# Kernel optimization log

Hardware: AMD Instinct MI355X
Metric: run time of the kernel (lower is better)

## Reference

```python
import jax, jax.numpy as jnp
import numpy as np
from jax import lax

K = 16
SIGMA2 = 1.0  # sigma=1.0 squared
EPS = 1e-06


def setup_inputs() -> dict:
    key = jax.random.key(0)
    xyz = jax.random.normal(key, (4, 3, 4096), dtype=jnp.float32)
    return {"xyz": xyz}


def reference(xyz):
    # xyz: (B, 3, N)
    B, _, N = xyz.shape
    pts = jnp.transpose(xyz, (0, 2, 1))  # (B, N, 3)

    sq = jnp.sum(pts * pts, axis=-1)  # (B, N)
    d2 = sq[:, :, None] + sq[:, None, :] - 2.0 * jnp.einsum("bnd,bmd->bnm", pts, pts)

    # k nearest neighbors (smallest distance, includes self like torch knn on same set)
    _, idx = lax.top_k(-d2, K)  # idx: (B, N, K)

    # gather neighbor coordinates and recompute exact squared distance (faithful to source)
    neighbors = jax.vmap(lambda p, i: p[i])(pts, idx)  # (B, N, K, 3)
    diff = pts[:, :, None, :] - neighbors
    dist2 = jnp.sum(diff * diff, axis=-1)  # (B, N, K)
    weights = jnp.exp(-dist2 / (2.0 * SIGMA2))

    # scatter k-sparse weights into dense adjacency (topk indices per row are unique)
    bb = jnp.arange(B)[:, None, None]
    ii = jnp.arange(N)[None, :, None]
    A = jnp.zeros((B, N, N), dtype=xyz.dtype).at[bb, ii, idx].set(weights)
    A = 0.5 * (A + jnp.swapaxes(A, 1, 2))

    # symmetric normalized Laplacian L = I - D^{-1/2} A D^{-1/2} (diag scaling via broadcast)
    D = jnp.clip(jnp.sum(A, axis=-1), EPS, None)
    d_is = D ** -0.5  # (B, N)
    L = jnp.eye(N, dtype=xyz.dtype)[None] - d_is[:, :, None] * A * d_is[:, None, :]
    return L
```

## Files before the change

kernel.cpp:

```cpp
#include <hip/hip_runtime.h>
#include <math.h>

#pragma clang fp contract(off)

#define NPTS 4096
#define KNN  16
#define RPBK 32
#define KT   1024
#define CAP  128
#define CAPIN 64
#define SPILLCAP 262144
#define RROWS 4

__device__ __forceinline__ unsigned okey(float f) {
    f = f + 0.0f;
    unsigned u = __float_as_uint(f);
    return u ^ (((unsigned)((int)u >> 31)) | 0x80000000u);
}

__device__ __forceinline__ unsigned long long wmin64(unsigned long long v) {
    for (int o = 32; o > 0; o >>= 1) { unsigned long long w = __shfl_xor(v, o); v = w < v ? w : v; }
    return v;
}

__global__ void zero_kernel(float* __restrict__ p, int n) {
    int i = blockIdx.x * blockDim.x + threadIdx.x;
    if (i < n) p[i] = 0.0f;
}

__device__ __forceinline__ float thresh16(float k, int lane) {
    int rank = 0;
    for (int s = 0; s < 64; ++s) {
        float ks = __shfl(k, s);
        rank += (ks < k || (ks == k && s < lane)) ? 1 : 0;
    }
    unsigned long long m = __ballot(rank == 15);
    return __shfl(k, __ffsll(m) - 1);
}

__device__ __forceinline__ int select16(const float4* __restrict__ spts,
                                        const int* __restrict__ list,
                                        int cnt, float4 P, int lane) {
    if (cnt <= 64) {
        float key = __builtin_huge_valf();
        int m = -1;
        if (lane < cnt) {
            m = list[lane];
            float4 Q = spts[m];
            float dot = (P.x * Q.x + P.y * Q.y) + P.z * Q.z;
            key = (P.w + Q.w) - 2.0f * dot;
        }
        int rank = 0;
        for (int s = 0; s < 64; ++s) {
            float ks = __shfl(key, s);
            rank += (ks < key || (ks == key && s < lane)) ? 1 : 0;
        }
        return __builtin_amdgcn_ds_permute(rank << 2, m);
    }
    if (cnt <= CAP) {
        unsigned long long e0 = ~0ull, e1 = ~0ull;
        if (lane < cnt) {
            int m = list[lane]; float4 Q = spts[m];
            float dot = (P.x * Q.x + P.y * Q.y) + P.z * Q.z;
            float d2  = (P.w + Q.w) - 2.0f * dot;
            e0 = ((unsigned long long)okey(d2) << 32) | (unsigned)m;
        }
        if (lane + 64 < cnt) {
            int m = list[lane + 64]; float4 Q = spts[m];
            float dot = (P.x * Q.x + P.y * Q.y) + P.z * Q.z;
            float d2  = (P.w + Q.w) - 2.0f * dot;
            e1 = ((unsigned long long)okey(d2) << 32) | (unsigned)m;
        }
        int selm = -1;
        unsigned long long c = e0 < e1 ? e0 : e1;
        for (int r = 0; r < KNN; ++r) {
            unsigned long long mn = wmin64(c);
            if (c == mn) {
                if (e0 == mn) e0 = ~0ull; else e1 = ~0ull;
                c = e0 < e1 ? e0 : e1;
            }
            if (lane == r) selm = (int)(unsigned)(mn & 0xFFFFFFFFull);
        }
        return selm;
    }
    unsigned long long last = 0; int selm = -1;
    for (int r = 0; r < KNN; ++r) {
        unsigned long long bestp = ~0ull;
        for (int i = 0; i < NPTS / 64; ++i) {
            int m = i * 64 + lane;
            float4 Q  = spts[m];
            float dot = (P.x * Q.x + P.y * Q.y) + P.z * Q.z;
            float d2  = (P.w + Q.w) - 2.0f * dot;
            unsigned long long key = ((unsigned long long)okey(d2) << 32) | (unsigned)m;
            if (key > last && key < bestp) bestp = key;
        }
        unsigned long long mn = wmin64(bestp);
        if (lane == r) selm = (int)(unsigned)(mn & 0xFFFFFFFFull);
        last = mn;
    }
    return selm;
}

__device__ __forceinline__ void emit_row(int rowg, int b, int selm, float4 P,
                                         const float4* __restrict__ spts,
                                         float* __restrict__ Dsum,
                                         int* __restrict__ idx_out,
                                         float* __restrict__ w_out,
                                         int* __restrict__ cnt,
                                         int* __restrict__ inc,
                                         int* __restrict__ spillc,
                                         int* __restrict__ spill,
                                         int do_inc, int lane) {
    float wgt = 0.0f;
    if (lane < KNN) {
        int j = selm;
        float4 Q = spts[j];
        float dx = P.x - Q.x, dy = P.y - Q.y, dz = P.z - Q.z;
        float dist2 = (dx * dx + dy * dy) + dz * dz;
        wgt = expf(-(dist2 * 0.5f));
        size_t base = (size_t)rowg * KNN + lane;
        idx_out[base] = j;
        w_out[base]   = wgt;
        int jg = (b << 12) + j;
        atomicAdd(&Dsum[jg], 0.5f * wgt);
        if (do_inc) {
            int pos = atomicAdd(&cnt[jg], 1);
            if (pos < CAPIN) {
                inc[(size_t)jg * CAPIN + pos] = (int)base;
            } else {
                int sp = atomicAdd(spillc, 1);
                if (sp < SPILLCAP) spill[sp] = (int)base;
            }
        }
    }
    float rs = wgt;
    for (int o = 32; o > 0; o >>= 1) rs += __shfl_xor(rs, o);
    if (lane == 0) atomicAdd(&Dsum[rowg], 0.5f * rs);
}

__global__ __launch_bounds__(KT, 4) void knn_kernel(const float* __restrict__ xyz,
                                                    float* __restrict__ Dsum,
                                                    int* __restrict__ idx_out,
                                                    float* __restrict__ w_out,
                                                    int* __restrict__ cnt,
                                                    int* __restrict__ inc,
                                                    int* __restrict__ spillc,
                                                    int* __restrict__ spill,
                                                    int do_inc) {
    __shared__ float4 spts[NPTS];
    __shared__ int    lists[RPBK][CAP];

    const int t    = threadIdx.x;
    const int lane = t & 63;
    const int wv   = t >> 6;
    const int row0 = blockIdx.x * RPBK + 2 * wv;
    const int b    = row0 >> 12;
    const float* X = xyz + (size_t)b * 3 * NPTS;

    for (int i = t; i < NPTS; i += KT) {
        float x = X[i], y = X[NPTS + i], z = X[2 * NPTS + i];
        spts[i] = make_float4(x, y, z, (x * x + y * y) + z * z);
    }
    __syncthreads();

    const float4 PA = spts[row0 & (NPTS - 1)];
    const float4 PB = spts[(row0 + 1) & (NPTS - 1)];

    float bA = __builtin_huge_valf(), bB = __builtin_huge_valf();
    for (int i = 0; i < NPTS / 64; ++i) {
        float4 Q  = spts[i * 64 + lane];
        float dotA = (PA.x * Q.x + PA.y * Q.y) + PA.z * Q.z;
        float d2A  = (PA.w + Q.w) - 2.0f * dotA;
        float dotB = (PB.x * Q.x + PB.y * Q.y) + PB.z * Q.z;
        float d2B  = (PB.w + Q.w) - 2.0f * dotB;
        bA = fminf(bA, d2A);
        bB = fminf(bB, d2B);
    }
    const float TA = thresh16(bA, lane);
    const float TB = thresh16(bB, lane);

    int* listA = &lists[2 * wv][0];
    int* listB = &lists[2 * wv + 1][0];
    int cA = 0, cB = 0;
    for (int i = 0; i < NPTS / 64; ++i) {
        int m = i * 64 + lane;
        float4 Q  = spts[m];
        float dotA = (PA.x * Q.x + PA.y * Q.y) + PA.z * Q.z;
        float d2A  = (PA.w + Q.w) - 2.0f * dotA;
        float dotB = (PB.x * Q.x + PB.y * Q.y) + PB.z * Q.z;
        float d2B  = (PB.w + Q.w) - 2.0f * dotB;
        bool pA = d2A <= TA;
        unsigned long long balA = __ballot(pA);
        if (pA) {
            int pos = cA + __popcll(balA & ((1ull << lane) - 1ull));
            if (pos < CAP) listA[pos] = m;
        }
        cA += (int)__popcll(balA);
        bool pB = d2B <= TB;
        unsigned long long balB = __ballot(pB);
        if (pB) {
            int pos = cB + __popcll(balB & ((1ull << lane) - 1ull));
            if (pos < CAP) listB[pos] = m;
        }
        cB += (int)__popcll(balB);
    }

    int selA = select16(spts, listA, cA, PA, lane);
    int selB = select16(spts, listB, cB, PB, lane);
    emit_row(row0,     b, selA, PA, spts, Dsum, idx_out, w_out,
             cnt, inc, spillc, spill, do_inc, lane);
    emit_row(row0 + 1, b, selB, PB, spts, Dsum, idx_out, w_out,
             cnt, inc, spillc, spill, do_inc, lane);
}

__global__ void dis_kernel(const float* __restrict__ Dsum, float* __restrict__ dis, int n) {
    int i = blockIdx.x * blockDim.x + threadIdx.x;
    if (i < n) dis[i] = 1.0f / sqrtf(fmaxf(Dsum[i], 1e-6f));
}

__global__ __launch_bounds__(1024, 4) void row_kernel(const int* __restrict__ idxb,
                                                      const float* __restrict__ wb,
                                                      const float* __restrict__ dis,
                                                      const int* __restrict__ cnt,
                                                      const int* __restrict__ inc,
                                                      float* __restrict__ L) {
    __shared__ float row[RROWS * NPTS];
    const int r0 = blockIdx.x * RROWS;
    const int b  = r0 >> 12;

    float4* row4 = (float4*)row;
    for (int i = threadIdx.x; i < RROWS * NPTS / 4; i += 1024)
        row4[i] = make_float4(0.0f, 0.0f, 0.0f, 0.0f);
    __syncthreads();

    const int rr = threadIdx.x >> 8;
    const int tt = threadIdx.x & 255;
    const int r  = r0 + rr;
    float* myrow = row + rr * NPTS;
    const float dn = dis[r];

    if (tt < KNN) {
        int g = r * KNN + tt;
        int j = idxb[g];
        float v = -0.5f * wb[g] * dn * dis[(b << 12) + j];
        atomicAdd(&myrow[j], v);
    }

    int c = cnt[r];
    if (c > CAPIN) c = CAPIN;
    for (int i = tt; i < c; i += 256) {
        int g   = inc[(size_t)r * CAPIN + i];
        int src = g >> 4;
        float v = -0.5f * wb[g] * dis[src] * dn;
        atomicAdd(&myrow[src & (NPTS - 1)], v);
    }
    __syncthreads();

    const int n0 = r0 & (NPTS - 1);
    float4* Lr = (float4*)(L + (size_t)b * NPTS * NPTS + (size_t)n0 * NPTS);
    for (int q = threadIdx.x; q < RROWS * NPTS / 4; q += 1024) {
        float4 v = row4[q];
        int n = n0 + (q >> 10);
        if ((q & 1023) == (n >> 2)) ((float*)&v)[n & 3] += 1.0f;
        Lr[q] = v;
    }
}

__global__ __launch_bounds__(256) void spill_kernel(const int* __restrict__ spillc,
                                                    const int* __restrict__ spill,
                                                    const int* __restrict__ idxb,
                                                    const float* __restrict__ wb,
                                                    const float* __restrict__ dis,
                                                    float* __restrict__ L) {
    int c = spillc[0];
    if (c > SPILLCAP) c = SPILLCAP;
    for (int i = blockIdx.x * blockDim.x + threadIdx.x; i < c;
         i += gridDim.x * blockDim.x) {
        int g   = spill[i];
        int src = g >> 4;
        int b   = src >> 12;
        int nn  = src & (NPTS - 1);
        int j   = idxb[g];
        float v = -0.5f * wb[g] * dis[src] * dis[(b << 12) + j];
        atomicAdd(L + (size_t)b * NPTS * NPTS + (size_t)j * NPTS + nn, v);
    }
}

__global__ __launch_bounds__(256) void fill_kernel(float4* __restrict__ L4, size_t T4) {
    size_t g4     = (size_t)blockIdx.x * blockDim.x + threadIdx.x;
    size_t stride = (size_t)gridDim.x * blockDim.x;
    for (; g4 < T4; g4 += stride) {
        size_t g = g4 << 2;
        int o    = (int)(g & (size_t)(NPTS * (size_t)NPTS - 1));
        int row  = o >> 12;
        int col0 = o & (NPTS - 1);
        float4 v;
        v.x = (row == col0    ) ? 1.0f : 0.0f;
        v.y = (row == col0 + 1) ? 1.0f : 0.0f;
        v.z = (row == col0 + 2) ? 1.0f : 0.0f;
        v.w = (row == col0 + 3) ? 1.0f : 0.0f;
        L4[g4] = v;
    }
}

__global__ __launch_bounds__(256) void scatter_kernel(const int* __restrict__ idxb,
                                                      const float* __restrict__ wb,
                                                      const float* __restrict__ dis,
                                                      float* __restrict__ L) {
    int g   = blockIdx.x * 256 + threadIdx.x;
    int row = g >> 4;
    int b   = row >> 12;
    int n   = row & (NPTS - 1);
    int j   = idxb[g];
    float v = -0.5f * wb[g] * dis[row] * dis[(b << 12) + j];
    float* Lb = L + (size_t)b * NPTS * NPTS;
    atomicAdd(Lb + (size_t)n * NPTS + j, v);
    atomicAdd(Lb + (size_t)j * NPTS + n, v);
}

extern "C" void kernel_launch(void* const* d_in, const int* in_sizes, int n_in,
                              void* d_out, int out_size, void* d_ws, size_t ws_size,
                              hipStream_t stream) {
    const float* xyz = (const float*)d_in[0];
    const int B  = in_sizes[0] / (3 * NPTS);
    const int BN = B * NPTS;

    float* Dsum   = (float*)d_ws;
    int*   cnt    = (int*)(Dsum + BN);
    int*   spillc = cnt + BN;
    float* dis    = (float*)(spillc + 16);
    int*   idxb   = (int*)(dis + BN);
    float* wb     = (float*)(idxb + (size_t)BN * KNN);
    int*   inc    = (int*)(wb + (size_t)BN * KNN);
    int*   spill  = inc + (size_t)BN * CAPIN;
    float* L      = (float*)d_out;

    size_t need = ((size_t)BN * (3 + 2 * KNN + CAPIN) + 16 + SPILLCAP) * 4;
    const int fused = (ws_size >= need);

    if (fused) {
        int nz = 2 * BN + 16;
        zero_kernel<<<(nz + 255) / 256, 256, 0, stream>>>(Dsum, nz);
        knn_kernel<<<BN / RPBK, KT, 0, stream>>>(xyz, Dsum, idxb, wb,
                                                 cnt, inc, spillc, spill, 1);
        dis_kernel<<<BN / 256, 256, 0, stream>>>(Dsum, dis, BN);
        row_kernel<<<BN / RROWS, 1024, 0, stream>>>(idxb, wb, dis, cnt, inc, L);
        spill_kernel<<<64, 256, 0, stream>>>(spillc, spill, idxb, wb, dis, L);
    } else {
        float* fDsum = (float*)d_ws;
        float* fdis  = fDsum + BN;
        int*   fidx  = (int*)(fdis + BN);
        float* fwb   = (float*)(fidx + (size_t)BN * KNN);
        zero_kernel<<<BN / 256, 256, 0, stream>>>(fDsum, BN);
        knn_kernel<<<BN / RPBK, KT, 0, stream>>>(xyz, fDsum, fidx, fwb,
                                                 nullptr, nullptr, nullptr, nullptr, 0);
        dis_kernel<<<BN / 256, 256, 0, stream>>>(fDsum, fdis, BN);
        size_t T4 = (size_t)B * NPTS * NPTS / 4;
        fill_kernel<<<8192, 256, 0, stream>>>((float4*)d_out, T4);
        scatter_kernel<<<(BN * KNN) / 256, 256, 0, stream>>>(fidx, fwb, fdis, L);
    }
}
```

Before: 340.2 us.

## Fuse knn, normalization, row build and spill into one persistent kernel with grid barriers

Merges the knn, degree-normalization, row-assembly and spill kernels into a single persistent kernel of 256 blocks that separates phases with atomic-counter grid barriers. It also raises rows per block in the row phase to 8, reusing one shared buffer across phases. The goal is to remove per-launch overhead and the tail gaps between the four launches. In exchange, the knn phase runs at most 256 blocks at once, so occupancy may be lower, and the grid barrier relies on all 256 blocks being resident at the same time.

```diff
diff --git a/kernel.cpp b/kernel.cpp
--- a/kernel.cpp
+++ b/kernel.cpp
@@ -6,11 +6,12 @@
 #define NPTS 4096
 #define KNN  16
 #define RPBK 32
-#define KT   1024
+#define MT   1024
+#define NBLK 256
 #define CAP  128
 #define CAPIN 64
 #define SPILLCAP 262144
-#define RROWS 4
+#define RROWS_C 8
 
 __device__ __forceinline__ unsigned okey(float f) {
     f = f + 0.0f;
@@ -23,7 +24,20 @@
     return v;
 }
 
-__global__ void zero_kernel(float* __restrict__ p, int n) {
+__device__ __forceinline__ void gridbar(unsigned* bar) {
+    __syncthreads();
+    if (threadIdx.x == 0) {
+        unsigned ticket = __hip_atomic_fetch_add(bar, 1u, __ATOMIC_ACQ_REL,
+                                                 __HIP_MEMORY_SCOPE_AGENT);
+        unsigned target = (ticket / NBLK + 1u) * NBLK;
+        while (__hip_atomic_load(bar, __ATOMIC_ACQUIRE,
+                                 __HIP_MEMORY_SCOPE_AGENT) < target)
+            __builtin_amdgcn_s_sleep(2);
+    }
+    __syncthreads();
+}
+
+__global__ void init_kernel(float* __restrict__ p, int n) {
     int i = blockIdx.x * blockDim.x + threadIdx.x;
     if (i < n) p[i] = 0.0f;
 }
@@ -138,15 +152,151 @@
     if (lane == 0) atomicAdd(&Dsum[rowg], 0.5f * rs);
 }
 
-__global__ __launch_bounds__(KT, 4) void knn_kernel(const float* __restrict__ xyz,
+__global__ __launch_bounds__(MT, 4) void mega_kernel(
+        const float* __restrict__ xyz,
+        float* __restrict__ Dsum, float* __restrict__ dis,
+        int* __restrict__ idxb, float* __restrict__ wb,
+        int* __restrict__ cnt, int* __restrict__ inc,
+        int* __restrict__ spillc, int* __restrict__ spill,
+        unsigned* __restrict__ bar, int BN, float* __restrict__ L) {
+    __shared__ __align__(16) char smem[RROWS_C * NPTS * 4];
+    float4* spts = (float4*)smem;
+    int (*lists)[CAP] = (int(*)[CAP])(smem + NPTS * 16);
+    float* rowbuf = (float*)smem;
+
+    const int t    = threadIdx.x;
+    const int bk   = blockIdx.x;
+    const int lane = t & 63;
+    const int wv   = t >> 6;
+
+    const int ngroups = BN / RPBK;
+    for (int g = bk; g < ngroups; g += NBLK) {
+        const int row0g = g * RPBK;
+        const int b     = row0g >> 12;
+        const float* X  = xyz + (size_t)b * 3 * NPTS;
+        __syncthreads();
+        for (int i = t; i < NPTS; i += MT) {
+            float x = X[i], y = X[NPTS + i], z = X[2 * NPTS + i];
+            spts[i] = make_float4(x, y, z, (x * x + y * y) + z * z);
+        }
+        __syncthreads();
+
+        const int row0 = row0g + 2 * wv;
+        const float4 PA = spts[row0 & (NPTS - 1)];
+        const float4 PB = spts[(row0 + 1) & (NPTS - 1)];
+
+        float bA = __builtin_huge_valf(), bB = __builtin_huge_valf();
+        for (int i = 0; i < NPTS / 64; ++i) {
+            float4 Q  = spts[i * 64 + lane];
+            float dotA = (PA.x * Q.x + PA.y * Q.y) + PA.z * Q.z;
+            float d2A  = (PA.w + Q.w) - 2.0f * dotA;
+            float dotB = (PB.x * Q.x + PB.y * Q.y) + PB.z * Q.z;
+            float d2B  = (PB.w + Q.w) - 2.0f * dotB;
+            bA = fminf(bA, d2A);
+            bB = fminf(bB, d2B);
+        }
+        const float TA = thresh16(bA, lane);
+        const float TB = thresh16(bB, lane);
+
+        int* listA = &lists[2 * wv][0];
+        int* listB = &lists[2 * wv + 1][0];
+        int cA = 0, cB = 0;
+        for (int i = 0; i < NPTS / 64; ++i) {
+            int m = i * 64 + lane;
+            float4 Q  = spts[m];
+            float dotA = (PA.x * Q.x + PA.y * Q.y) + PA.z * Q.z;
+            float d2A  = (PA.w + Q.w) - 2.0f * dotA;
+            float dotB = (PB.x * Q.x + PB.y * Q.y) + PB.z * Q.z;
+            float d2B  = (PB.w + Q.w) - 2.0f * dotB;
+            bool pA = d2A <= TA;
+            unsigned long long balA = __ballot(pA);
+            if (pA) {
+                int pos = cA + __popcll(balA & ((1ull << lane) - 1ull));
+                if (pos < CAP) listA[pos] = m;
+            }
+            cA += (int)__popcll(balA);
+            bool pB = d2B <= TB;
+            unsigned long long balB = __ballot(pB);
+            if (pB) {
+                int pos = cB + __popcll(balB & ((1ull << lane) - 1ull));
+                if (pos < CAP) listB[pos] = m;
+            }
+            cB += (int)__popcll(balB);
+        }
+
+        int selA = select16(spts, listA, cA, PA, lane);
+        int selB = select16(spts, listB, cB, PB, lane);
+        emit_row(row0,     b, selA, PA, spts, Dsum, idxb, wb,
+                 cnt, inc, spillc, spill, 1, lane);
+        emit_row(row0 + 1, b, selB, PB, spts, Dsum, idxb, wb,
+                 cnt, inc, spillc, spill, 1, lane);
+    }
+    gridbar(bar);
+
+    for (int i = bk * MT + t; i < BN; i += NBLK * MT)
+        dis[i] = 1.0f / sqrtf(fmaxf(Dsum[i], 1e-6f));
+    gridbar(bar);
+
+    const int rows_per_blk = BN / NBLK;
+    float4* row4 = (float4*)rowbuf;
+    for (int it = 0; it < rows_per_blk / RROWS_C; ++it) {
+        const int r0 = bk * rows_per_blk + it * RROWS_C;
+        const int b0 = r0 >> 12;
+
+        for (int i = t; i < RROWS_C * NPTS / 4; i += MT)
+            row4[i] = make_float4(0.0f, 0.0f, 0.0f, 0.0f);
+        __syncthreads();
+
+        const int rr = t >> 7;
+        const int tt = t & 127;
+        const int r  = r0 + rr;
+        float* myrow = rowbuf + rr * NPTS;
+        const float dn = dis[r];
+
+        if (tt < KNN) {
+            int g = r * KNN + tt;
+            int j = idxb[g];
+            float v = -0.5f * wb[g] * dn * dis[(b0 << 12) + j];
+            atomicAdd(&myrow[j], v);
+        }
+        int c = cnt[r];
+        if (c > CAPIN) c = CAPIN;
+        for (int i = tt; i < c; i += 128) {
+            int g   = inc[(size_t)r * CAPIN + i];
+            int src = g >> 4;
+            float v = -0.5f * wb[g] * dis[src] * dn;
+            atomicAdd(&myrow[src & (NPTS - 1)], v);
+        }
+        __syncthreads();
+
+        const int n0 = r0 & (NPTS - 1);
+        float4* Lr = (float4*)(L + (size_t)b0 * NPTS * NPTS + (size_t)n0 * NPTS);
+        for (int q = t; q < RROWS_C * NPTS / 4; q += MT) {
+            float4 v = row4[q];
+            int n = n0 + (q >> 10);
+            if ((q & 1023) == (n >> 2)) ((float*)&v)[n & 3] += 1.0f;
+            Lr[q] = v;
+        }
+    }
+    gridbar(bar);
+
+    int c = spillc[0];
+    if (c > SPILLCAP) c = SPILLCAP;
+    for (int i = bk * MT + t; i < c; i += NBLK * MT) {
+        int g   = spill[i];
+        int src = g >> 4;
+        int b   = src >> 12;
+        int nn  = src & (NPTS - 1);
+        int j   = idxb[g];
+        float v = -0.5f * wb[g] * dis[src] * dis[(b << 12) + j];
+        atomicAdd(L + (size_t)b * NPTS * NPTS + (size_t)j * NPTS + nn, v);
+    }
+}
+
+__global__ __launch_bounds__(MT, 4) void knn_kernel(const float* __restrict__ xyz,
                                                     float* __restrict__ Dsum,
                                                     int* __restrict__ idx_out,
-                                                    float* __restrict__ w_out,
-                                                    int* __restrict__ cnt,
-                                                    int* __restrict__ inc,
-                                                    int* __restrict__ spillc,
-                                                    int* __restrict__ spill,
-                                                    int do_inc) {
+                                                    float* __restrict__ w_out) {
     __shared__ float4 spts[NPTS];
     __shared__ int    lists[RPBK][CAP];
 
@@ -157,7 +307,7 @@
     const int b    = row0 >> 12;
     const float* X = xyz + (size_t)b * 3 * NPTS;
 
-    for (int i = t; i < NPTS; i += KT) {
+    for (int i = t; i < NPTS; i += MT) {
         float x = X[i], y = X[NPTS + i], z = X[2 * NPTS + i];
         spts[i] = make_float4(x, y, z, (x * x + y * y) + z * z);
     }
@@ -165,7 +315,6 @@
 
     const float4 PA = spts[row0 & (NPTS - 1)];
     const float4 PB = spts[(row0 + 1) & (NPTS - 1)];
-
     float bA = __builtin_huge_valf(), bB = __builtin_huge_valf();
     for (int i = 0; i < NPTS / 64; ++i) {
         float4 Q  = spts[i * 64 + lane];
@@ -178,7 +327,6 @@
     }
     const float TA = thresh16(bA, lane);
     const float TB = thresh16(bB, lane);
-
     int* listA = &lists[2 * wv][0];
     int* listB = &lists[2 * wv + 1][0];
     int cA = 0, cB = 0;
@@ -204,86 +352,17 @@
         }
         cB += (int)__popcll(balB);
     }
-
     int selA = select16(spts, listA, cA, PA, lane);
     int selB = select16(spts, listB, cB, PB, lane);
     emit_row(row0,     b, selA, PA, spts, Dsum, idx_out, w_out,
-             cnt, inc, spillc, spill, do_inc, lane);
+             nullptr, nullptr, nullptr, nullptr, 0, lane);
     emit_row(row0 + 1, b, selB, PB, spts, Dsum, idx_out, w_out,
-             cnt, inc, spillc, spill, do_inc, lane);
+             nullptr, nullptr, nullptr, nullptr, 0, lane);
 }
 
 __global__ void dis_kernel(const float* __restrict__ Dsum, float* __restrict__ dis, int n) {
     int i = blockIdx.x * blockDim.x + threadIdx.x;
     if (i < n) dis[i] = 1.0f / sqrtf(fmaxf(Dsum[i], 1e-6f));
-}
-
-__global__ __launch_bounds__(1024, 4) void row_kernel(const int* __restrict__ idxb,
-                                                      const float* __restrict__ wb,
-                                                      const float* __restrict__ dis,
-                                                      const int* __restrict__ cnt,
-                                                      const int* __restrict__ inc,
-                                                      float* __restrict__ L) {
-    __shared__ float row[RROWS * NPTS];
-    const int r0 = blockIdx.x * RROWS;
-    const int b  = r0 >> 12;
-
-    float4* row4 = (float4*)row;
-    for (int i = threadIdx.x; i < RROWS * NPTS / 4; i += 1024)
-        row4[i] = make_float4(0.0f, 0.0f, 0.0f, 0.0f);
-    __syncthreads();
-
-    const int rr = threadIdx.x >> 8;
-    const int tt = threadIdx.x & 255;
-    const int r  = r0 + rr;
-    float* myrow = row + rr * NPTS;
-    const float dn = dis[r];
-
-    if (tt < KNN) {
-        int g = r * KNN + tt;
-        int j = idxb[g];
-        float v = -0.5f * wb[g] * dn * dis[(b << 12) + j];
-        atomicAdd(&myrow[j], v);
-    }
-
-    int c = cnt[r];
-    if (c > CAPIN) c = CAPIN;
-    for (int i = tt; i < c; i += 256) {
-        int g   = inc[(size_t)r * CAPIN + i];
-        int src = g >> 4;
-        float v = -0.5f * wb[g] * dis[src] * dn;
-        atomicAdd(&myrow[src & (NPTS - 1)], v);
-    }
-    __syncthreads();
-
-    const int n0 = r0 & (NPTS - 1);
-    float4* Lr = (float4*)(L + (size_t)b * NPTS * NPTS + (size_t)n0 * NPTS);
-    for (int q = threadIdx.x; q < RROWS * NPTS / 4; q += 1024) {
-        float4 v = row4[q];
-        int n = n0 + (q >> 10);
-        if ((q & 1023) == (n >> 2)) ((float*)&v)[n & 3] += 1.0f;
-        Lr[q] = v;
-    }
-}
-
-__global__ __launch_bounds__(256) void spill_kernel(const int* __restrict__ spillc,
-                                                    const int* __restrict__ spill,
-                                                    const int* __restrict__ idxb,
-                                                    const float* __restrict__ wb,
-                                                    const float* __restrict__ dis,
-                                                    float* __restrict__ L) {
-    int c = spillc[0];
-    if (c > SPILLCAP) c = SPILLCAP;
-    for (int i = blockIdx.x * blockDim.x + threadIdx.x; i < c;
-         i += gridDim.x * blockDim.x) {
-        int g   = spill[i];
-        int src = g >> 4;
-        int b   = src >> 12;
-        int nn  = src & (NPTS - 1);
-        int j   = idxb[g];
-        float v = -0.5f * wb[g] * dis[src] * dis[(b << 12) + j];
-        atomicAdd(L + (size_t)b * NPTS * NPTS + (size_t)j * NPTS + nn, v);
-    }
 }
 
 __global__ __launch_bounds__(256) void fill_kernel(float4* __restrict__ L4, size_t T4) {
@@ -325,35 +404,33 @@
     const int B  = in_sizes[0] / (3 * NPTS);
     const int BN = B * NPTS;
 
-    float* Dsum   = (float*)d_ws;
-    int*   cnt    = (int*)(Dsum + BN);
-    int*   spillc = cnt + BN;
-    float* dis    = (float*)(spillc + 16);
-    int*   idxb   = (int*)(dis + BN);
-    float* wb     = (float*)(idxb + (size_t)BN * KNN);
-    int*   inc    = (int*)(wb + (size_t)BN * KNN);
-    int*   spill  = inc + (size_t)BN * CAPIN;
-    float* L      = (float*)d_out;
-
-    size_t need = ((size_t)BN * (3 + 2 * KNN + CAPIN) + 16 + SPILLCAP) * 4;
+    float*    Dsum   = (float*)d_ws;
+    int*      cnt    = (int*)(Dsum + BN);
+    int*      spillc = cnt + BN;
+    unsigned* bar    = (unsigned*)(spillc + 16);
+    float*    dis    = (float*)(bar + 16);
+    int*      idxb   = (int*)(dis + BN);
+    float*    wb     = (float*)(idxb + (size_t)BN * KNN);
+    int*      inc    = (int*)(wb + (size_t)BN * KNN);
+    int*      spill  = inc + (size_t)BN * CAPIN;
+    float*    L      = (float*)d_out;
+
+    size_t need = ((size_t)BN * (3 + 2 * KNN + CAPIN) + 32 + SPILLCAP) * 4;
     const int fused = (ws_size >= need);
 
     if (fused) {
-        int nz = 2 * BN + 16;
-        zero_kernel<<<(nz + 255) / 256, 256, 0, stream>>>(Dsum, nz);
-        knn_kernel<<<BN / RPBK, KT, 0, stream>>>(xyz, Dsum, idxb, wb,
-                                                 cnt, inc, spillc, spill, 1);
-        dis_kernel<<<BN / 256, 256, 0, stream>>>(Dsum, dis, BN);
-        row_kernel<<<BN / RROWS, 1024, 0, stream>>>(idxb, wb, dis, cnt, inc, L);
-        spill_kernel<<<64, 256, 0, stream>>>(spillc, spill, idxb, wb, dis, L);
+        int nz = 2 * BN + 32;
+        init_kernel<<<(nz + 255) / 256, 256, 0, stream>>>(Dsum, nz);
+        mega_kernel<<<NBLK, MT, 0, stream>>>(xyz, Dsum, dis, idxb, wb,
+                                             cnt, inc, spillc, spill,
+                                             bar, BN, L);
     } else {
         float* fDsum = (float*)d_ws;
         float* fdis  = fDsum + BN;
         int*   fidx  = (int*)(fdis + BN);
         float* fwb   = (float*)(fidx + (size_t)BN * KNN);
-        zero_kernel<<<BN / 256, 256, 0, stream>>>(fDsum, BN);
-        knn_kernel<<<BN / RPBK, KT, 0, stream>>>(xyz, fDsum, fidx, fwb,
-                                                 nullptr, nullptr, nullptr, nullptr, 0);
+        init_kernel<<<BN / 256, 256, 0, stream>>>(fDsum, BN);
+        knn_kernel<<<BN / RPBK, MT, 0, stream>>>(xyz, fDsum, fidx, fwb);
         dis_kernel<<<BN / 256, 256, 0, stream>>>(fDsum, fdis, BN);
         size_t T4 = (size_t)B * NPTS * NPTS / 4;
         fill_kernel<<<8192, 256, 0, stream>>>((float4*)d_out, T4);
```

Result: slower. 456.0 us (+34.0%).

## Precompute point float4s globally and process four rows per wave in KNN

Applied to the files above, without the earlier changes.

A prep kernel now builds packed (x,y,z,|p|^2) points once in global memory and also zeroes the accumulators, replacing the zero kernel. The KNN kernel no longer stages all 4096 points into shared memory per block. It uses 256-thread blocks with each wave handling four rows, so every loaded point is reused across four distance computations. The candidate list cap drops to 64, which removes the 65–128 selection path, so rows with more candidates fall back to the slow full-scan selection. Points are now read through global/L2 instead of LDS, which cuts per-block LDS fill work and raises occupancy but adds cache traffic.

```diff
diff --git a/kernel.cpp b/kernel.cpp
--- a/kernel.cpp
+++ b/kernel.cpp
@@ -5,9 +5,11 @@
 
 #define NPTS 4096
 #define KNN  16
-#define RPBK 32
-#define KT   1024
-#define CAP  128
+#define RW   4
+#define KWAVES 4
+#define KBT  256
+#define KROWS (KWAVES * RW)
+#define CAP  64
 #define CAPIN 64
 #define SPILLCAP 262144
 #define RROWS 4
@@ -23,9 +25,18 @@
     return v;
 }
 
-__global__ void zero_kernel(float* __restrict__ p, int n) {
-    int i = blockIdx.x * blockDim.x + threadIdx.x;
-    if (i < n) p[i] = 0.0f;
+__global__ __launch_bounds__(256) void prep_kernel(const float* __restrict__ xyz,
+                                                   float4* __restrict__ pts4,
+                                                   float* __restrict__ zbuf,
+                                                   int nzero, int BN) {
+    int i = blockIdx.x * 256 + threadIdx.x;
+    if (i < BN) {
+        int b = i >> 12, n = i & (NPTS - 1);
+        const float* X = xyz + (size_t)b * 3 * NPTS;
+        float x = X[n], y = X[NPTS + n], z = X[2 * NPTS + n];
+        pts4[i] = make_float4(x, y, z, (x * x + y * y) + z * z);
+    }
+    if (i < nzero) zbuf[i] = 0.0f;
 }
 
 __device__ __forceinline__ float thresh16(float k, int lane) {
@@ -38,15 +49,15 @@
     return __shfl(k, __ffsll(m) - 1);
 }
 
-__device__ __forceinline__ int select16(const float4* __restrict__ spts,
+__device__ __forceinline__ int select16(const float4* __restrict__ pts,
                                         const int* __restrict__ list,
-                                        int cnt, float4 P, int lane) {
-    if (cnt <= 64) {
+                                        int cnt2, float4 P, int lane) {
+    if (cnt2 <= 64) {
         float key = __builtin_huge_valf();
         int m = -1;
-        if (lane < cnt) {
+        if (lane < cnt2) {
             m = list[lane];
-            float4 Q = spts[m];
+            float4 Q = pts[m];
             float dot = (P.x * Q.x + P.y * Q.y) + P.z * Q.z;
             key = (P.w + Q.w) - 2.0f * dot;
         }
@@ -56,39 +67,13 @@
             rank += (ks < key || (ks == key && s < lane)) ? 1 : 0;
         }
         return __builtin_amdgcn_ds_permute(rank << 2, m);
-    }
-    if (cnt <= CAP) {
-        unsigned long long e0 = ~0ull, e1 = ~0ull;
-        if (lane < cnt) {
-            int m = list[lane]; float4 Q = spts[m];
-            float dot = (P.x * Q.x + P.y * Q.y) + P.z * Q.z;
-            float d2  = (P.w + Q.w) - 2.0f * dot;
-            e0 = ((unsigned long long)okey(d2) << 32) | (unsigned)m;
-        }
-        if (lane + 64 < cnt) {
-            int m = list[lane + 64]; float4 Q = spts[m];
-            float dot = (P.x * Q.x + P.y * Q.y) + P.z * Q.z;
-            float d2  = (P.w + Q.w) - 2.0f * dot;
-            e1 = ((unsigned long long)okey(d2) << 32) | (unsigned)m;
-        }
-        int selm = -1;
-        unsigned long long c = e0 < e1 ? e0 : e1;
-        for (int r = 0; r < KNN; ++r) {
-            unsigned long long mn = wmin64(c);
-            if (c == mn) {
-                if (e0 == mn) e0 = ~0ull; else e1 = ~0ull;
-                c = e0 < e1 ? e0 : e1;
-            }
-            if (lane == r) selm = (int)(unsigned)(mn & 0xFFFFFFFFull);
-        }
-        return selm;
     }
     unsigned long long last = 0; int selm = -1;
     for (int r = 0; r < KNN; ++r) {
         unsigned long long bestp = ~0ull;
         for (int i = 0; i < NPTS / 64; ++i) {
             int m = i * 64 + lane;
-            float4 Q  = spts[m];
+            float4 Q  = pts[m];
             float dot = (P.x * Q.x + P.y * Q.y) + P.z * Q.z;
             float d2  = (P.w + Q.w) - 2.0f * dot;
             unsigned long long key = ((unsigned long long)okey(d2) << 32) | (unsigned)m;
@@ -102,7 +87,7 @@
 }
 
 __device__ __forceinline__ void emit_row(int rowg, int b, int selm, float4 P,
-                                         const float4* __restrict__ spts,
+                                         const float4* __restrict__ pts,
                                          float* __restrict__ Dsum,
                                          int* __restrict__ idx_out,
                                          float* __restrict__ w_out,
@@ -114,7 +99,7 @@
     float wgt = 0.0f;
     if (lane < KNN) {
         int j = selm;
-        float4 Q = spts[j];
+        float4 Q = pts[j];
         float dx = P.x - Q.x, dy = P.y - Q.y, dz = P.z - Q.z;
         float dist2 = (dx * dx + dy * dy) + dz * dz;
         wgt = expf(-(dist2 * 0.5f));
@@ -138,79 +123,69 @@
     if (lane == 0) atomicAdd(&Dsum[rowg], 0.5f * rs);
 }
 
-__global__ __launch_bounds__(KT, 4) void knn_kernel(const float* __restrict__ xyz,
-                                                    float* __restrict__ Dsum,
-                                                    int* __restrict__ idx_out,
-                                                    float* __restrict__ w_out,
-                                                    int* __restrict__ cnt,
-                                                    int* __restrict__ inc,
-                                                    int* __restrict__ spillc,
-                                                    int* __restrict__ spill,
-                                                    int do_inc) {
-    __shared__ float4 spts[NPTS];
-    __shared__ int    lists[RPBK][CAP];
+__global__ __launch_bounds__(KBT, 4) void knn_kernel(const float4* __restrict__ pts4,
+                                                     float* __restrict__ Dsum,
+                                                     int* __restrict__ idx_out,
+                                                     float* __restrict__ w_out,
+                                                     int* __restrict__ cnt,
+                                                     int* __restrict__ inc,
+                                                     int* __restrict__ spillc,
+                                                     int* __restrict__ spill,
+                                                     int do_inc) {
+    __shared__ int lists[KROWS][CAP];
 
     const int t    = threadIdx.x;
     const int lane = t & 63;
     const int wv   = t >> 6;
-    const int row0 = blockIdx.x * RPBK + 2 * wv;
+    const int row0 = blockIdx.x * KROWS + wv * RW;
     const int b    = row0 >> 12;
-    const float* X = xyz + (size_t)b * 3 * NPTS;
-
-    for (int i = t; i < NPTS; i += KT) {
-        float x = X[i], y = X[NPTS + i], z = X[2 * NPTS + i];
-        spts[i] = make_float4(x, y, z, (x * x + y * y) + z * z);
-    }
-    __syncthreads();
-
-    const float4 PA = spts[row0 & (NPTS - 1)];
-    const float4 PB = spts[(row0 + 1) & (NPTS - 1)];
-
-    float bA = __builtin_huge_valf(), bB = __builtin_huge_valf();
+    const float4* P4 = pts4 + ((size_t)b << 12);
+
+    float4 P[RW]; float bm[RW];
+#pragma unroll
+    for (int r = 0; r < RW; ++r) {
+        P[r]  = P4[(row0 + r) & (NPTS - 1)];
+        bm[r] = __builtin_huge_valf();
+    }
+
+#pragma unroll 4
     for (int i = 0; i < NPTS / 64; ++i) {
-        float4 Q  = spts[i * 64 + lane];
-        float dotA = (PA.x * Q.x + PA.y * Q.y) + PA.z * Q.z;
-        float d2A  = (PA.w + Q.w) - 2.0f * dotA;
-        float dotB = (PB.x * Q.x + PB.y * Q.y) + PB.z * Q.z;
-        float d2B  = (PB.w + Q.w) - 2.0f * dotB;
-        bA = fminf(bA, d2A);
-        bB = fminf(bB, d2B);
-    }
-    const float TA = thresh16(bA, lane);
-    const float TB = thresh16(bB, lane);
-
-    int* listA = &lists[2 * wv][0];
-    int* listB = &lists[2 * wv + 1][0];
-    int cA = 0, cB = 0;
+        float4 Q = P4[i * 64 + lane];
+#pragma unroll
+        for (int r = 0; r < RW; ++r) {
+            float dot = (P[r].x * Q.x + P[r].y * Q.y) + P[r].z * Q.z;
+            float d2  = (P[r].w + Q.w) - 2.0f * dot;
+            bm[r] = fminf(bm[r], d2);
+        }
+    }
+    float T[RW]; int cc[RW];
+#pragma unroll
+    for (int r = 0; r < RW; ++r) { T[r] = thresh16(bm[r], lane); cc[r] = 0; }
+
+#pragma unroll 2
     for (int i = 0; i < NPTS / 64; ++i) {
         int m = i * 64 + lane;
-        float4 Q  = spts[m];
-        float dotA = (PA.x * Q.x + PA.y * Q.y) + PA.z * Q.z;
-        float d2A  = (PA.w + Q.w) - 2.0f * dotA;
-        float dotB = (PB.x * Q.x + PB.y * Q.y) + PB.z * Q.z;
-        float d2B  = (PB.w + Q.w) - 2.0f * dotB;
-        bool pA = d2A <= TA;
-        unsigned long long balA = __ballot(pA);
-        if (pA) {
-            int pos = cA + __popcll(balA & ((1ull << lane) - 1ull));
-            if (pos < CAP) listA[pos] = m;
-        }
-        cA += (int)__popcll(balA);
-        bool pB = d2B <= TB;
-        unsigned long long balB = __ballot(pB);
-        if (pB) {
-            int pos = cB + __popcll(balB & ((1ull << lane) - 1ull));
-            if (pos < CAP) listB[pos] = m;
-        }
-        cB += (int)__popcll(balB);
-    }
-
-    int selA = select16(spts, listA, cA, PA, lane);
-    int selB = select16(spts, listB, cB, PB, lane);
-    emit_row(row0,     b, selA, PA, spts, Dsum, idx_out, w_out,
-             cnt, inc, spillc, spill, do_inc, lane);
-    emit_row(row0 + 1, b, selB, PB, spts, Dsum, idx_out, w_out,
-             cnt, inc, spillc, spill, do_inc, lane);
+        float4 Q = P4[m];
+#pragma unroll
+        for (int r = 0; r < RW; ++r) {
+            float dot = (P[r].x * Q.x + P[r].y * Q.y) + P[r].z * Q.z;
+            float d2  = (P[r].w + Q.w) - 2.0f * dot;
+            bool pass = d2 <= T[r];
+            unsigned long long bal = __ballot(pass);
+            if (pass) {
+                int pos = cc[r] + __popcll(bal & ((1ull << lane) - 1ull));
+                if (pos < CAP) lists[wv * RW + r][pos] = m;
+            }
+            cc[r] += (int)__popcll(bal);
+        }
+    }
+
+#pragma unroll
+    for (int r = 0; r < RW; ++r) {
+        int sel = select16(P4, &lists[wv * RW + r][0], cc[r], P[r], lane);
+        emit_row(row0 + r, b, sel, P[r], P4, Dsum, idx_out, w_out,
+                 cnt, inc, spillc, spill, do_inc, lane);
+    }
 }
 
 __global__ void dis_kernel(const float* __restrict__ Dsum, float* __restrict__ dis, int n) {
@@ -245,7 +220,6 @@
         float v = -0.5f * wb[g] * dn * dis[(b << 12) + j];
         atomicAdd(&myrow[j], v);
     }
-
     int c = cnt[r];
     if (c > CAPIN) c = CAPIN;
     for (int i = tt; i < c; i += 256) {
@@ -325,35 +299,38 @@
     const int B  = in_sizes[0] / (3 * NPTS);
     const int BN = B * NPTS;
 
-    float* Dsum   = (float*)d_ws;
-    int*   cnt    = (int*)(Dsum + BN);
-    int*   spillc = cnt + BN;
-    float* dis    = (float*)(spillc + 16);
-    int*   idxb   = (int*)(dis + BN);
-    float* wb     = (float*)(idxb + (size_t)BN * KNN);
-    int*   inc    = (int*)(wb + (size_t)BN * KNN);
-    int*   spill  = inc + (size_t)BN * CAPIN;
-    float* L      = (float*)d_out;
-
-    size_t need = ((size_t)BN * (3 + 2 * KNN + CAPIN) + 16 + SPILLCAP) * 4;
+    float4* pts4   = (float4*)d_ws;
+    float*  Dsum   = (float*)(pts4 + BN);
+    int*    cnt    = (int*)(Dsum + BN);
+    int*    spillc = cnt + BN;
+    float*  dis    = (float*)(spillc + 16);
+    int*    idxb   = (int*)(dis + BN);
+    float*  wb     = (float*)(idxb + (size_t)BN * KNN);
+    int*    inc    = (int*)(wb + (size_t)BN * KNN);
+    int*    spill  = inc + (size_t)BN * CAPIN;
+    float*  L      = (float*)d_out;
+
+    size_t need = ((size_t)BN * (4 + 3 + 2 * KNN + CAPIN) + 16 + SPILLCAP) * 4;
     const int fused = (ws_size >= need);
 
     if (fused) {
         int nz = 2 * BN + 16;
-        zero_kernel<<<(nz + 255) / 256, 256, 0, stream>>>(Dsum, nz);
-        knn_kernel<<<BN / RPBK, KT, 0, stream>>>(xyz, Dsum, idxb, wb,
-                                                 cnt, inc, spillc, spill, 1);
+        int mx = nz > BN ? nz : BN;
+        prep_kernel<<<(mx + 255) / 256, 256, 0, stream>>>(xyz, pts4, Dsum, nz, BN);
+        knn_kernel<<<BN / KROWS, KBT, 0, stream>>>(pts4, Dsum, idxb, wb,
+                                                   cnt, inc, spillc, spill, 1);
         dis_kernel<<<BN / 256, 256, 0, stream>>>(Dsum, dis, BN);
         row_kernel<<<BN / RROWS, 1024, 0, stream>>>(idxb, wb, dis, cnt, inc, L);
         spill_kernel<<<64, 256, 0, stream>>>(spillc, spill, idxb, wb, dis, L);
     } else {
-        float* fDsum = (float*)d_ws;
-        float* fdis  = fDsum + BN;
-        int*   fidx  = (int*)(fdis + BN);
-        float* fwb   = (float*)(fidx + (size_t)BN * KNN);
-        zero_kernel<<<BN / 256, 256, 0, stream>>>(fDsum, BN);
-        knn_kernel<<<BN / RPBK, KT, 0, stream>>>(xyz, fDsum, fidx, fwb,
-                                                 nullptr, nullptr, nullptr, nullptr, 0);
+        float4* fpts  = (float4*)d_ws;
+        float*  fDsum = (float*)(fpts + BN);
+        float*  fdis  = fDsum + BN;
+        int*    fidx  = (int*)(fdis + BN);
+        float*  fwb   = (float*)(fidx + (size_t)BN * KNN);
+        prep_kernel<<<(BN + 255) / 256, 256, 0, stream>>>(xyz, fpts, fDsum, BN, BN);
+        knn_kernel<<<BN / KROWS, KBT, 0, stream>>>(fpts, fDsum, fidx, fwb,
+                                                   nullptr, nullptr, nullptr, nullptr, 0);
         dis_kernel<<<BN / 256, 256, 0, stream>>>(fDsum, fdis, BN);
         size_t T4 = (size_t)B * NPTS * NPTS / 4;
         fill_kernel<<<8192, 256, 0, stream>>>((float4*)d_out, T4);
```

New measurement: 369.9 us. +8.7%, slower.
